# Optimization experiments

Hardware: AMD Instinct MI355X
Metric: run time of the kernel (lower is better)

The kernel has to match this reference:

```python
import jax, jax.numpy as jnp
import numpy as np

B, N, T, F, K = 32, 24, 12, 3, 3
COUT = 12                      # must equal T (LayerNorm applied to last dim = T)
DIN = N * COUT + N + 1         # 313 = lstm_in_dim
H = DIN * T                    # 3756 = lstm_hidden_dim (forced by residual add)
ODIM = 1
LN_EPS = 1e-5


def setup_inputs() -> dict:
    key = jax.random.key(0)
    ks = jax.random.split(key, 24)
    r = lambda i, shape, s=0.1: jax.random.normal(ks[i], shape, dtype=jnp.float32) * s
    return {
        "X": r(0, (B, N, T, F), 1.0),
        "cheb": r(1, (K, N, N), 0.3),
        # Spatial_Attention_layer (ASTGCN-style) params
        "sa_W1": r(2, (T,)), "sa_W2": r(3, (F, T)), "sa_W3": r(4, (F,)),
        "sa_bs": r(5, (1, N, N)), "sa_Vs": r(6, (N, N)),
        # Temporal_Attention_layer params
        "ta_U1": r(7, (N,)), "ta_U2": r(8, (F, N)), "ta_U3": r(9, (F,)),
        "ta_be": r(10, (1, T, T)), "ta_Ve": r(11, (T, T)),
        # ChebConv_with_sa params
        "theta": r(12, (K, F, COUT)), "cheb_bias": jnp.zeros((COUT,), jnp.float32),
        # LayerNorm
        "ln_g": jnp.ones((COUT,), jnp.float32), "ln_b": jnp.zeros((COUT,), jnp.float32),
        # layer_in: Linear(seq_len, seq_len)
        "layer_in_w": r(13, (T, T)), "layer_in_b": r(14, (T,)),
        # S_A2: Linear(lstm_in_dim, lstm_in_dim)
        "sa2_w": r(15, (DIN, DIN), 0.05), "sa2_b": r(16, (DIN,)),
        # LSTMCell (torch gate order i,f,g,o)
        "W_ih": r(17, (4 * H, DIN), 0.02), "W_hh": r(18, (4 * H, H), 0.01),
        "b_ih": jnp.zeros((4 * H,), jnp.float32), "b_hh": jnp.zeros((4 * H,), jnp.float32),
        # T_A2: Linear(seq_len*hidden, seq_len)
        "ta2_w": r(19, (T, T * H), 0.02), "ta2_b": r(20, (T,)),
        # layer_out
        "out_w": r(21, (ODIM, H), 0.02), "out_b": jnp.zeros((ODIM,), jnp.float32),
        # torch.randn initial states (fixed here for determinism)
        "h0": r(22, (B, H), 1.0), "c0": r(23, (B, H), 1.0),
    }


def reference(X, cheb, sa_W1, sa_W2, sa_W3, sa_bs, sa_Vs,
              ta_U1, ta_U2, ta_U3, ta_be, ta_Ve,
              theta, cheb_bias, ln_g, ln_b,
              layer_in_w, layer_in_b, sa2_w, sa2_b,
              W_ih, W_hh, b_ih, b_hh, ta2_w, ta2_b,
              out_w, out_b, h0, c0):
    sig = jax.nn.sigmoid
    Bsz = X.shape[0]
    x_flow = X[:, 0:1, :, 1]                     # (B,1,T)
    x_rain = X[:, :, :, 0]                       # (B,N,T)
    x_pre = jnp.concatenate([x_rain, x_flow], axis=1)  # (B,N+1,T)
    x4 = jnp.transpose(X, (0, 1, 3, 2))          # (B,N,F,T)

    # spatial attention; legacy nn.Softmax() on 3D tensor => axis=0
    lhs = jnp.einsum('bnf,ft->bnt', jnp.einsum('bnft,t->bnf', x4, sa_W1), sa_W2)
    rhs = jnp.einsum('f,bnft->btn', sa_W3, x4)
    S = jnp.einsum('nm,bmk->bnk', sa_Vs, sig(jnp.einsum('bnt,btm->bnm', lhs, rhs) + sa_bs))
    s_a = jax.nn.softmax(sig(jax.nn.softmax(S, axis=1)), axis=0)   # (B,N,N)

    # temporal attention
    xp = jnp.transpose(x4, (0, 3, 2, 1))         # (B,T,F,N)
    lhs_t = jnp.einsum('btf,fn->btn', jnp.einsum('btfn,n->btf', xp, ta_U1), ta_U2)
    rhs_t = jnp.einsum('f,bnft->bnt', ta_U3, x4)
    E = jnp.einsum('tu,buv->btv', ta_Ve, sig(jnp.einsum('btn,bnu->btu', lhs_t, rhs_t) + ta_be))
    t_a = jax.nn.softmax(sig(jax.nn.softmax(E, axis=1)), axis=0)   # (B,T,T)

    # attention-weighted Chebyshev conv; note reshape (not transpose), as in original
    xg = X.reshape(Bsz, N, F, -1)                # (B,N,F,T)
    Tk_at = cheb[None] * s_a[:, None]            # (B,K,N,N)
    rhs_g = jnp.einsum('bkmn,bmft->bknft', Tk_at, xg)
    xc = jax.nn.relu(jnp.einsum('bknft,kfo->bnot', rhs_g, theta) + cheb_bias[:, None])  # (B,N,COUT,T)

    # LayerNorm over last dim (T == COUT)
    mu = xc.mean(-1, keepdims=True)
    var = xc.var(-1, keepdims=True)
    x_ln = (xc - mu) / jnp.sqrt(var + LN_EPS) * ln_g + ln_b

    x_gc = x_ln.reshape(Bsz, -1, 12)             # (B, N*COUT, 12)
    x_gc_t = jnp.einsum('bij,bjk->bik', x_gc, t_a)
    x_res = jnp.concatenate([x_gc_t, x_pre], axis=1)   # (B, DIN, 12)
    x_in = x_res @ layer_in_w.T + layer_in_b     # Linear over last (seq) dim
    xs = jnp.transpose(x_in, (2, 0, 1))          # (T, B, DIN)

    def step(carry, x_t):
        h, c = carry
        alpha = jax.nn.softmax(sig(x_t @ sa2_w.T + sa2_b), axis=1)
        xi = x_t * alpha + x_t
        gates = xi @ W_ih.T + b_ih + h @ W_hh.T + b_hh
        i, f, g, o = jnp.split(gates, 4, axis=1)
        c2 = sig(f) * c + sig(i) * jnp.tanh(g)
        h2 = sig(o) * jnp.tanh(c2)
        return (h2, c2), h2

    _, hs = jax.lax.scan(step, (h0, c0), xs)     # (T,B,H)
    total_ht = jnp.transpose(hs, (1, 0, 2)).reshape(Bsz, -1)  # cat along dim 1, time-major
    beta = jax.nn.softmax(jax.nn.relu(total_ht @ ta2_w.T + ta2_b), axis=1)  # (B,T)
    out = jnp.einsum('tbh,bt->bh', hs, beta)
    out = out + x_in.reshape(Bsz, -1)            # requires H == DIN*T
    out = jax.nn.relu(out) @ out_w.T + out_b
    return out, s_a
```

## Files before the change

kernel.cpp:

```cpp
#include <hip/hip_runtime.h>

#define BSZ 32
#define NN 24
#define TT 12
#define FF 3
#define KK 3
#define COUT 12
#define DIN 313
#define HID 3756
#define H4 15024
#define KP 3776
#define KPI 320
#define NTILES 470
#define NB 235
#define NCH 30

using short8 = __attribute__((ext_vector_type(8))) short;
using f32x4  = __attribute__((ext_vector_type(4))) float;

__device__ inline unsigned short f2bf(float f){
  union{float f; unsigned u;} v; v.f=f;
  unsigned u=v.u;
  return (unsigned short)((u + 0x7FFFu + ((u>>16)&1u))>>16);
}
__device__ inline f32x4 mfma16(short8 a, short8 b, f32x4 c){
  return __builtin_amdgcn_mfma_f32_16x16x32_bf16(a,b,c,0,0,0);
}
__device__ inline float sigm(float x){ return 1.f/(1.f+expf(-x)); }

__device__ void conv_slab(const float* __restrict__ W, unsigned short* __restrict__ Wp,
    int bi, int cg0, int cg1, int tid, int nthr, unsigned short* lds){
  for(int cg=cg0; cg<cg1; cg++){
    int ks0=cg*4;
    int nks=min(4,118-ks0);
    int nf4=nks*8;
    for(int q=tid;q<64*nf4;q+=nthr){
      int r=q/nf4, f4=q-r*nf4;
      int g=r>>4, lj=r&15;
      int jj=bi*16+lj; if(jj>=HID) jj=HID-1;
      const float* src=W+(long)(g*HID+jj)*HID;
      int k=ks0*32+f4*4;
      ushort4 o;
      if(k+3<HID){
        float4 v=*(const float4*)(src+k);
        o.x=f2bf(v.x); o.y=f2bf(v.y); o.z=f2bf(v.z); o.w=f2bf(v.w);
      } else {
        float vv[4];
        #pragma unroll
        for(int t2=0;t2<4;t2++){ int kk=k+t2; vv[t2]=(kk<HID)?src[kk]:0.f; }
        o.x=f2bf(vv[0]); o.y=f2bf(vv[1]); o.z=f2bf(vv[2]); o.w=f2bf(vv[3]);
      }
      *(ushort4*)(&lds[r*136+f4*4])=o;
    }
    __syncthreads();
    for(int idx=tid; idx<nks*4*64; idx+=nthr){
      int l=idx&63, g=(idx>>6)&3, kl=idx>>8;
      int lj=l&15, lk=l>>4;
      short8 v=*(short8*)(&lds[(g*16+lj)*136 + kl*32 + lk*8]);
      *(short8*)(Wp + (((long)(bi*118+ks0+kl)*4+g)*64 + l)*8) = v;
    }
    __syncthreads();
  }
}

__device__ void pack_ih(const float* __restrict__ Wih, unsigned short* __restrict__ Wip,
    int jt, int tid, int nthr, unsigned short* lds ){
  int j0=jt*32;
  for(int q=tid;q<32*80;q+=nthr){
    int r=q/80, f4=q-r*80;
    int j=j0+r;
    int k=f4*4;
    ushort4 o;
    if(j<H4){
      const float* src=Wih+(long)j*DIN;
      float vv[4];
      #pragma unroll
      for(int t2=0;t2<4;t2++){ int kk=k+t2; vv[t2]=(kk<DIN)?src[kk]:0.f; }
      o.x=f2bf(vv[0]); o.y=f2bf(vv[1]); o.z=f2bf(vv[2]); o.w=f2bf(vv[3]);
    } else { o.x=0;o.y=0;o.z=0;o.w=0; }
    *(ushort4*)(&lds[r*328+k])=o;
  }
  __syncthreads();
  for(int u=tid;u<1280;u+=nthr){
    int l=u&63, jh=(u>>6)&1, ks=u>>7;
    int lj=l&15, lk=l>>4;
    short8 v=*(short8*)(&lds[(jh*16+lj)*328 + ks*32 + lk*8]);
    *(short8*)(Wip + (((long)(jt*10+ks)*2+jh)*512) + l*8)=v;
  }
  __syncthreads();
}

__global__ void __launch_bounds__(256) k_f1(const float* __restrict__ X,
   const float* __restrict__ sa_W1, const float* __restrict__ sa_W2,
   const float* __restrict__ sa_W3, const float* __restrict__ sa_bs,
   const float* __restrict__ sa_Vs, const float* __restrict__ ta_U1,
   const float* __restrict__ ta_U2, const float* __restrict__ ta_U3,
   const float* __restrict__ ta_be, const float* __restrict__ ta_Ve,
   float* __restrict__ SA_pre, float* __restrict__ TA_pre,
   const float* __restrict__ W, unsigned short* __restrict__ Wp,
   const float* __restrict__ Wih, unsigned short* __restrict__ Wip){
  __shared__ __align__(16) float smf[5248];
  int tid=threadIdx.x;
  if(blockIdx.x>=267){
    int cb=blockIdx.x-267;
    #pragma unroll
    for(int s=0;s<4;s++){
      int jt=cb*4+s;
      if(jt<NTILES) pack_ih(Wih,Wip,jt,tid,256,(unsigned short*)smf);
    }
    return;
  }
  if(blockIdx.x>=32){
    conv_slab(W,Wp,blockIdx.x-32,0,8,tid,256,(unsigned short*)smf);
    return;
  }
  int b=blockIdx.x;
  float* lin=smf;        float* lhs=smf+864;   float* rhs=smf+1152;
  float* P=smf+1440;     float* S=smf+2016;    float* lhsT=smf+2592;
  float* rhsT=smf+2880;  float* PT=smf+3168;   float* E=smf+3312;
  for(int i=tid;i<864;i+=256) lin[i]=X[b*864+i];
  __syncthreads();
  for(int i=tid;i<NN*TT;i+=256){ int n=i/TT, t=i%TT;
    float acc=0;
    #pragma unroll
    for(int f=0;f<FF;f++){
      float t1=0;
      for(int u=0;u<TT;u++) t1 += lin[n*36+u*3+f]*sa_W1[u];
      acc += t1*sa_W2[f*TT+t];
    }
    lhs[n*TT+t]=acc;
    float r=0;
    #pragma unroll
    for(int f=0;f<FF;f++) r += sa_W3[f]*lin[n*36+t*3+f];
    rhs[t*NN+n]=r;
  }
  for(int i=tid;i<TT*NN;i+=256){ int t=i/NN, n=i%NN;
    float acc=0;
    #pragma unroll
    for(int f=0;f<FF;f++){
      float t1=0;
      for(int m=0;m<NN;m++) t1 += lin[m*36+t*3+f]*ta_U1[m];
      acc += t1*ta_U2[f*NN+n];
    }
    lhsT[t*NN+n]=acc;
    float r=0;
    #pragma unroll
    for(int f=0;f<FF;f++) r += ta_U3[f]*lin[n*36+t*3+f];
    rhsT[n*TT+t]=r;
  }
  __syncthreads();
  for(int i=tid;i<NN*NN;i+=256){ int n=i/NN,m=i%NN;
    float a=0;
    for(int t=0;t<TT;t++) a+=lhs[n*TT+t]*rhs[t*NN+m];
    P[i]=sigm(a+sa_bs[i]);
  }
  for(int i=tid;i<TT*TT;i+=256){ int t=i/TT,u=i%TT;
    float a=0;
    for(int n=0;n<NN;n++) a+=lhsT[t*NN+n]*rhsT[n*TT+u];
    PT[i]=sigm(a+ta_be[i]);
  }
  __syncthreads();
  for(int i=tid;i<NN*NN;i+=256){ int n=i/NN,k=i%NN;
    float a=0;
    for(int m=0;m<NN;m++) a+=sa_Vs[n*NN+m]*P[m*NN+k];
    S[i]=a;
  }
  for(int i=tid;i<TT*TT;i+=256){ int t=i/TT,v=i%TT;
    float a=0;
    for(int u=0;u<TT;u++) a+=ta_Ve[t*TT+u]*PT[u*TT+v];
    E[i]=a;
  }
  __syncthreads();
  if(tid<NN){ int k=tid;
    float mx=-1e30f;
    for(int n=0;n<NN;n++) mx=fmaxf(mx,S[n*NN+k]);
    float sm=0;
    for(int n=0;n<NN;n++) sm+=__expf(S[n*NN+k]-mx);
    for(int n=0;n<NN;n++){
      float v=__expf(S[n*NN+k]-mx)/sm;
      SA_pre[b*576+n*NN+k]=sigm(v);
    }
  }
  if(tid>=32 && tid<32+TT){ int v=tid-32;
    float mx=-1e30f;
    for(int t=0;t<TT;t++) mx=fmaxf(mx,E[t*TT+v]);
    float sm=0;
    for(int t=0;t<TT;t++) sm+=__expf(E[t*TT+v]-mx);
    for(int t=0;t<TT;t++){
      float e=__expf(E[t*TT+v]-mx)/sm;
      TA_pre[b*144+t*TT+v]=sigm(e);
    }
  }
}

__global__ void __launch_bounds__(320) k_f2(const float* __restrict__ X,
  const float* __restrict__ cheb, const float* __restrict__ SA_pre,
  const float* __restrict__ TA_pre, const float* __restrict__ theta,
  const float* __restrict__ cheb_bias, const float* __restrict__ ln_g,
  const float* __restrict__ ln_b, const float* __restrict__ liw,
  const float* __restrict__ lib, float* __restrict__ x_in,
  float* __restrict__ out_sa,
  const float* __restrict__ W, unsigned short* __restrict__ Wp,
  const float* __restrict__ sa2_w, float* __restrict__ sa2_wT){
  __shared__ __align__(16) float smf[13116];
  int tid=threadIdx.x;
  if(blockIdx.x>=267){
    int cb=blockIdx.x-267;
    for(int idx=cb*320+tid; idx<DIN*DIN; idx+=40*320){
      int i=idx/DIN, j=idx-i*DIN;
      sa2_wT[idx]=sa2_w[(long)j*DIN+i];
    }
    return;
  }
  if(blockIdx.x>=32){
    conv_slab(W,Wp,blockIdx.x-32,8,16,tid,320,(unsigned short*)smf);
    return;
  }
  int b=blockIdx.x;
  float* lin =smf;
  float* A2  =smf+864;
  float* rg  =smf+2592;
  float* xc  =smf+5184;
  float* xres=smf+8640;
  float* tal =smf+12396;
  float* sa_l=smf+12540;
  for(int i=tid;i<864;i+=320) lin[i]=X[b*864+i];
  for(int i=tid;i<576;i+=320){
    float mx=-1e30f;
    for(int bb=0;bb<BSZ;bb++) mx=fmaxf(mx,SA_pre[bb*576+i]);
    float sm=0;
    for(int bb=0;bb<BSZ;bb++) sm+=__expf(SA_pre[bb*576+i]-mx);
    float v=__expf(SA_pre[b*576+i]-mx)/sm;
    sa_l[i]=v;
    out_sa[b*576+i]=v;
  }
  for(int i=tid;i<144;i+=320){
    float mx=-1e30f;
    for(int bb=0;bb<BSZ;bb++) mx=fmaxf(mx,TA_pre[bb*144+i]);
    float sm=0;
    for(int bb=0;bb<BSZ;bb++) sm+=__expf(TA_pre[bb*144+i]-mx);
    tal[i]=__expf(TA_pre[b*144+i]-mx)/sm;
  }
  __syncthreads();
  for(int i=tid;i<KK*NN*NN;i+=320){ int mn=i%576; A2[i]=cheb[i]*sa_l[mn]; }
  __syncthreads();
  for(int i=tid;i<KK*NN*FF*TT;i+=320){
    int t=i%TT, f=(i/TT)%FF, n=(i/36)%NN, k=i/864;
    float a=0;
    for(int m=0;m<NN;m++) a+=A2[k*576+m*NN+n]*lin[m*36+f*TT+t];
    rg[i]=a;
  }
  __syncthreads();
  for(int i=tid;i<NN*COUT*TT;i+=320){
    int t=i%TT, o=(i/TT)%COUT, n=i/(COUT*TT);
    float a=cheb_bias[o];
    #pragma unroll
    for(int k=0;k<KK;k++)
      #pragma unroll
      for(int f=0;f<FF;f++)
        a += rg[((k*NN+n)*FF+f)*TT+t]*theta[(k*FF+f)*COUT+o];
    xc[i]=fmaxf(a,0.f);
  }
  __syncthreads();
  if(tid<NN*COUT){
    float mu=0;
    for(int t=0;t<TT;t++) mu+=xc[tid*TT+t];
    mu*=(1.f/12.f);
    float var=0;
    for(int t=0;t<TT;t++){ float d=xc[tid*TT+t]-mu; var+=d*d; }
    var*=(1.f/12.f);
    float inv=rsqrtf(var+1e-5f);
    for(int t=0;t<TT;t++) xc[tid*TT+t]=(xc[tid*TT+t]-mu)*inv*ln_g[t]+ln_b[t];
  }
  __syncthreads();
  for(int i=tid;i<NN*COUT;i+=320){
    for(int v=0;v<TT;v++){
      float a=0;
      for(int t=0;t<TT;t++) a+=xc[i*TT+t]*tal[t*TT+v];
      xres[i*TT+v]=a;
    }
  }
  for(int i=tid;i<25*TT;i+=320){
    int r=i/TT, t=i%TT;
    float v=(r<NN)? lin[r*36+t*3+0] : lin[t*3+1];
    xres[(288+r)*TT+t]=v;
  }
  __syncthreads();
  for(int i=tid;i<DIN;i+=320){
    for(int t=0;t<TT;t++){
      float a=lib[t];
      #pragma unroll
      for(int u=0;u<TT;u++) a+=xres[i*TT+u]*liw[t*TT+u];
      x_in[((long)b*DIN+i)*TT+t]=a;
    }
  }
}

__global__ void __launch_bounds__(512) k_f3(const float* __restrict__ x_in,
    const float* __restrict__ sa2_wT, const float* __restrict__ sa2_b,
    unsigned short* __restrict__ xi_b,
    const float* __restrict__ W, unsigned short* __restrict__ Wp){
  __shared__ __align__(16) float smf[4352];
  int tid=threadIdx.x;
  if(blockIdx.x>=384){
    conv_slab(W,Wp,blockIdx.x-384,16,23,tid,512,(unsigned short*)smf);
    return;
  }
  int blk=blockIdx.x; int t=blk>>5, b=blk&31;
  float* xt=smf;
  float* red=smf+320;
  if(tid<DIN) xt[tid]=x_in[((long)b*DIN+tid)*TT+t];
  __syncthreads();
  float z=-1e30f, e=0.f;
  if(tid<DIN){
    float a=sa2_b[tid];
    for(int i=0;i<DIN;i++) a+=xt[i]*sa2_wT[(long)i*DIN+tid];
    z=sigm(a);
  }
  red[tid]=z; __syncthreads();
  for(int off=256;off>0;off>>=1){ if(tid<off) red[tid]=fmaxf(red[tid],red[tid+off]); __syncthreads(); }
  float mx=red[0]; __syncthreads();
  e=(tid<DIN)?__expf(z-mx):0.f;
  red[tid]=e; __syncthreads();
  for(int off=256;off>0;off>>=1){ if(tid<off) red[tid]+=red[tid+off]; __syncthreads(); }
  float sm=red[0];
  if(tid<KPI){
    unsigned short v=0;
    if(tid<DIN){
      float alpha=e/sm;
      v=f2bf(xt[tid]*alpha+xt[tid]);
    }
    xi_b[(long)blk*KPI+tid]=v;
  }
}

__global__ void __launch_bounds__(256) k_f4(const unsigned short* __restrict__ xi,
   const unsigned short* __restrict__ Wip, const float* __restrict__ b_ih,
   const float* __restrict__ b_hh, float* __restrict__ Gx,
   const float* __restrict__ W, unsigned short* __restrict__ Wp,
   const float* __restrict__ h0f, unsigned short* __restrict__ hb0,
   unsigned short* __restrict__ hb1){
  __shared__ __align__(16) float smf[4352];
  int tid=threadIdx.x;
  if(blockIdx.x>=118){
    int cb_=blockIdx.x-118;
    conv_slab(W,Wp,cb_,23,30,tid,256,(unsigned short*)smf);
    const int g4=KP>>2;
    for(int i=cb_*256+tid; i<BSZ*g4; i+=NB*256){
      int gq=i%g4, r=i/g4;
      int k=gq*4;
      float vv[4];
      if(k+3<HID){
        float4 x=*(const float4*)(h0f+(long)r*HID+k);
        vv[0]=x.x; vv[1]=x.y; vv[2]=x.z; vv[3]=x.w;
      } else {
        #pragma unroll
        for(int q=0;q<4;q++){ int kk=k+q; vv[q]=(kk<HID)? h0f[(long)r*HID+kk] : 0.f; }
      }
      ushort4 o;
      o.x=f2bf(vv[0]); o.y=f2bf(vv[1]); o.z=f2bf(vv[2]); o.w=f2bf(vv[3]);
      *(ushort4*)(hb0+(long)r*KP+k)=o;
      *(ushort4*)(hb1+(long)r*KP+k)=o;
    }
    return;
  }
  int w=tid>>6, lane=tid&63;
  int jt=blockIdx.x*4+w;
  if(jt>=NTILES) return;
  int j0=jt*32;
  int lj=lane&15, lk=lane>>4;
  const unsigned short* wslab = Wip + (long)jt*10240;
  short8 bfr[10][2];
  #pragma unroll
  for(int ks=0;ks<10;ks++)
    #pragma unroll
    for(int jh=0;jh<2;jh++)
      bfr[ks][jh]=*(const short8*)(wslab + ((ks*2+jh)<<9) + (lane<<3));
  for(int t=0;t<TT;t++){
    f32x4 acc[2][2]={};
    #pragma unroll
    for(int ks=0;ks<10;ks++){
      #pragma unroll
      for(int mh=0;mh<2;mh++){
        short8 a=*(const short8*)(xi + ((long)(t*32+mh*16+lj))*KPI + ks*32 + lk*8);
        acc[mh][0]=mfma16(a,bfr[ks][0],acc[mh][0]);
        acc[mh][1]=mfma16(a,bfr[ks][1],acc[mh][1]);
      }
    }
    #pragma unroll
    for(int mh=0;mh<2;mh++)
      #pragma unroll
      for(int jh=0;jh<2;jh++){
        int j=j0+jh*16+lj;
        if(j<H4){
          float bias=b_ih[j]+b_hh[j];
          #pragma unroll
          for(int r=0;r<4;r++){
            int bb=mh*16+lk*4+r;
            Gx[((long)t*32+bb)*H4+j]=acc[mh][jh][r]+bias;
          }
        }
      }
  }
}

__global__ void __launch_bounds__(512) k_step(const unsigned short* __restrict__ hb_r,
    unsigned short* __restrict__ hb_w, const unsigned short* __restrict__ Wp,
    const float* __restrict__ Gx, const float* __restrict__ c0,
    float* __restrict__ c, float* __restrict__ hs, int t){
  const int tid=threadIdx.x;
  const int w=tid>>6, lane=tid&63;
  const int j0=blockIdx.x*16;
  const int lj=lane&15, lk=lane>>4;
  const int s0=(118*w)>>3, s1=(118*(w+1))>>3;
  const unsigned short* slab = Wp + (long)blockIdx.x*64*KP;
  f32x4 acc[4][2]={};
  #pragma unroll 2
  for(int ks=s0;ks<s1;ks++){
    int kofs=ks*32+lk*8;
    short8 a0=*(const short8*)(hb_r + (long)lj*KP + kofs);
    short8 a1=*(const short8*)(hb_r + (long)(16+lj)*KP + kofs);
    const unsigned short* pk = slab + ((long)ks<<11);
    #pragma unroll
    for(int g=0;g<4;g++){
      short8 bv=*(const short8*)(pk + (g<<9) + (lane<<3));
      acc[g][0]=mfma16(a0,bv,acc[g][0]);
      acc[g][1]=mfma16(a1,bv,acc[g][1]);
    }
  }
  __shared__ float red[8][4][512];
  #pragma unroll
  for(int g=0;g<4;g++)
    #pragma unroll
    for(int mh=0;mh<2;mh++)
      #pragma unroll
      for(int r=0;r<4;r++)
        red[w][g][(mh*16+lk*4+r)*16+lj]=acc[g][mh][r];
  __syncthreads();
  if(tid<512){
    int p=tid;
    int bb=p>>4, jl=p&15; int j=j0+jl;
    if(j<HID){
      long gxo=((long)t*BSZ+bb)*H4 + j;
      float si=0,sf=0,sg=0,so=0;
      #pragma unroll
      for(int ww=0;ww<8;ww++){
        si+=red[ww][0][p]; sf+=red[ww][1][p];
        sg+=red[ww][2][p]; so+=red[ww][3][p];
      }
      si+=Gx[gxo]; sf+=Gx[gxo+HID]; sg+=Gx[gxo+2*HID]; so+=Gx[gxo+3*HID];
      float gi=sigm(si), gf=sigm(sf), gg=tanhf(sg), go=sigm(so);
      int idx=bb*HID+j;
      float cin=(t==0)?c0[idx]:c[idx];
      float c2=gf*cin+gi*gg;
      float h2=go*tanhf(c2);
      c[idx]=c2;
      hs[(long)t*BSZ*HID+idx]=h2;
      hb_w[(long)bb*KP+j]=f2bf(h2);
    }
  }
}

__global__ void k_tail(const float* __restrict__ hs, const float* __restrict__ ta2_w,
   const float* __restrict__ ta2_b, const float* __restrict__ x_in,
   const float* __restrict__ out_w, const float* __restrict__ out_b,
   float* __restrict__ out0){
  int b=blockIdx.x, tid=threadIdx.x;
  float p[12]={0,0,0,0,0,0,0,0,0,0,0,0};
  for(int idx=tid; idx<TT*HID; idx+=256){
    int t=idx/HID, j=idx-t*HID;
    float v=hs[((long)t*BSZ+b)*HID+j];
    #pragma unroll
    for(int q=0;q<12;q++) p[q]+=v*ta2_w[(long)q*TT*HID+idx];
  }
  __shared__ float red[256];
  __shared__ float bt[12];
  float z[12];
  #pragma unroll
  for(int q=0;q<12;q++){
    __syncthreads();
    red[tid]=p[q]; __syncthreads();
    for(int off=128;off>0;off>>=1){ if(tid<off) red[tid]+=red[tid+off]; __syncthreads(); }
    z[q]=red[0];
  }
  if(tid==0){
    float mx=-1e30f;
    #pragma unroll
    for(int q=0;q<12;q++){ z[q]=fmaxf(z[q]+ta2_b[q],0.f); mx=fmaxf(mx,z[q]); }
    float sm=0;
    #pragma unroll
    for(int q=0;q<12;q++){ z[q]=__expf(z[q]-mx); sm+=z[q]; }
    #pragma unroll
    for(int q=0;q<12;q++) bt[q]=z[q]/sm;
  }
  __syncthreads();
  float acc=0;
  for(int j=tid;j<HID;j+=256){
    float ov=0;
    #pragma unroll
    for(int t=0;t<TT;t++) ov+=hs[((long)t*BSZ+b)*HID+j]*bt[t];
    ov+=x_in[(long)b*HID+j];
    acc+=fmaxf(ov,0.f)*out_w[j];
  }
  __syncthreads();
  red[tid]=acc; __syncthreads();
  for(int off=128;off>0;off>>=1){ if(tid<off) red[tid]+=red[tid+off]; __syncthreads(); }
  if(tid==0) out0[b]=red[0]+out_b[0];
}

extern "C" void kernel_launch(void* const* d_in, const int* in_sizes, int n_in,
                              void* d_out, int out_size, void* d_ws, size_t ws_size,
                              hipStream_t stream){
  (void)in_sizes; (void)n_in; (void)out_size; (void)ws_size;
  const float* X     =(const float*)d_in[0];
  const float* cheb  =(const float*)d_in[1];
  const float* sa_W1 =(const float*)d_in[2];
  const float* sa_W2 =(const float*)d_in[3];
  const float* sa_W3 =(const float*)d_in[4];
  const float* sa_bs =(const float*)d_in[5];
  const float* sa_Vs =(const float*)d_in[6];
  const float* ta_U1 =(const float*)d_in[7];
  const float* ta_U2 =(const float*)d_in[8];
  const float* ta_U3 =(const float*)d_in[9];
  const float* ta_be =(const float*)d_in[10];
  const float* ta_Ve =(const float*)d_in[11];
  const float* theta =(const float*)d_in[12];
  const float* cb    =(const float*)d_in[13];
  const float* ln_g  =(const float*)d_in[14];
  const float* ln_b  =(const float*)d_in[15];
  const float* liw   =(const float*)d_in[16];
  const float* lib   =(const float*)d_in[17];
  const float* sa2_w =(const float*)d_in[18];
  const float* sa2_b =(const float*)d_in[19];
  const float* W_ih  =(const float*)d_in[20];
  const float* W_hh  =(const float*)d_in[21];
  const float* b_ih  =(const float*)d_in[22];
  const float* b_hh  =(const float*)d_in[23];
  const float* ta2_w =(const float*)d_in[24];
  const float* ta2_b =(const float*)d_in[25];
  const float* out_w =(const float*)d_in[26];
  const float* out_b =(const float*)d_in[27];
  const float* h0    =(const float*)d_in[28];
  const float* c0    =(const float*)d_in[29];

  char* w=(char*)d_ws;
  unsigned short* Wp =(unsigned short*)(w);
  float* Gx   =(float*)(w+113582080);
  float* hs   =(float*)(w+136658944);
  unsigned short* hb0=(unsigned short*)(w+142428160);
  unsigned short* hb1=(unsigned short*)(w+142669824);
  float* c    =(float*)(w+142911488);
  float* x_in =(float*)(w+143392256);
  unsigned short* xi_b=(unsigned short*)(w+143873024);
  float* SA   =(float*)(w+144118784);
  float* TA   =(float*)(w+144192512);
  unsigned short* Wip=(unsigned short*)(w+144211968);
  float* sa2T =(float*)(w+153837568);
  float* out_f=(float*)d_out;

  k_f1<<<385,256,0,stream>>>(X,sa_W1,sa_W2,sa_W3,sa_bs,sa_Vs,ta_U1,ta_U2,ta_U3,ta_be,ta_Ve,
                             SA,TA,W_hh,Wp,W_ih,Wip);
  k_f2<<<307,320,0,stream>>>(X,cheb,SA,TA,theta,cb,ln_g,ln_b,liw,lib,x_in,out_f+32,W_hh,Wp,
                             sa2_w,sa2T);
  k_f3<<<384+NB,512,0,stream>>>(x_in,sa2T,sa2_b,xi_b,W_hh,Wp);
  k_f4<<<118+NB,256,0,stream>>>(xi_b,Wip,b_ih,b_hh,Gx,W_hh,Wp,h0,hb0,hb1);
  unsigned short* hb[2]={hb0,hb1};
  for(int t=0;t<TT;t++)
    k_step<<<NB,512,0,stream>>>(hb[t&1],hb[(t+1)&1],Wp,Gx,c0,c,hs,t);
  k_tail<<<32,256,0,stream>>>(hs,ta2_w,ta2_b,x_in,out_w,out_b,out_f);
}
```

Before: 555.6 us.

## Split per-batch graph-conv kernel into per-(batch,node) blocks plus separate layer_in kernel

The preprocessing kernel previously used one block per batch (32 blocks) for the Chebyshev conv, LayerNorm and temporal attention chain. It is now split into 768 blocks, one per (batch, node), which write an intermediate xres buffer. A new elementwise kernel then applies the layer_in linear. The aim is to fill more compute units and shorten this serial stage, at the cost of an extra kernel launch, a global round-trip for xres, and redundant per-block loads of X and the attention softmax.

Result: no change. 564.0 us (+1.5%).

```diff
diff --git a/kernel.cpp b/kernel.cpp
--- a/kernel.cpp
+++ b/kernel.cpp
@@ -193,48 +193,45 @@
   }
 }
 
-__global__ void __launch_bounds__(320) k_f2(const float* __restrict__ X,
+__global__ void __launch_bounds__(256) k_f2a(const float* __restrict__ X,
   const float* __restrict__ cheb, const float* __restrict__ SA_pre,
   const float* __restrict__ TA_pre, const float* __restrict__ theta,
   const float* __restrict__ cheb_bias, const float* __restrict__ ln_g,
-  const float* __restrict__ ln_b, const float* __restrict__ liw,
-  const float* __restrict__ lib, float* __restrict__ x_in,
+  const float* __restrict__ ln_b, float* __restrict__ xres,
   float* __restrict__ out_sa,
   const float* __restrict__ W, unsigned short* __restrict__ Wp,
   const float* __restrict__ sa2_w, float* __restrict__ sa2_wT){
-  __shared__ __align__(16) float smf[13116];
+  __shared__ __align__(16) float smf[4352];
   int tid=threadIdx.x;
-  if(blockIdx.x>=267){
-    int cb=blockIdx.x-267;
-    for(int idx=cb*320+tid; idx<DIN*DIN; idx+=40*320){
+  if(blockIdx.x>=1003){
+    int cb=blockIdx.x-1003;
+    for(int idx=cb*256+tid; idx<DIN*DIN; idx+=40*256){
       int i=idx/DIN, j=idx-i*DIN;
       sa2_wT[idx]=sa2_w[(long)j*DIN+i];
     }
     return;
   }
-  if(blockIdx.x>=32){
-    conv_slab(W,Wp,blockIdx.x-32,8,16,tid,320,(unsigned short*)smf);
+  if(blockIdx.x>=768){
+    conv_slab(W,Wp,blockIdx.x-768,8,16,tid,256,(unsigned short*)smf);
     return;
   }
-  int b=blockIdx.x;
-  float* lin =smf;
-  float* A2  =smf+864;
-  float* rg  =smf+2592;
-  float* xc  =smf+5184;
-  float* xres=smf+8640;
-  float* tal =smf+12396;
-  float* sa_l=smf+12540;
-  for(int i=tid;i<864;i+=320) lin[i]=X[b*864+i];
-  for(int i=tid;i<576;i+=320){
+  int b=blockIdx.x/NN, n=blockIdx.x%NN;
+  float* lin=smf;
+  float* tal=smf+864;
+  float* sal=smf+1008;
+  float* rg =smf+1032;
+  float* xc =smf+1140;
+  for(int i=tid;i<864;i+=256) lin[i]=X[b*864+i];
+  if(tid<NN){ int m=tid; int mn=m*NN+n;
     float mx=-1e30f;
-    for(int bb=0;bb<BSZ;bb++) mx=fmaxf(mx,SA_pre[bb*576+i]);
+    for(int bb=0;bb<BSZ;bb++) mx=fmaxf(mx,SA_pre[bb*576+mn]);
     float sm=0;
-    for(int bb=0;bb<BSZ;bb++) sm+=__expf(SA_pre[bb*576+i]-mx);
-    float v=__expf(SA_pre[b*576+i]-mx)/sm;
-    sa_l[i]=v;
-    out_sa[b*576+i]=v;
-  }
-  for(int i=tid;i<144;i+=320){
+    for(int bb=0;bb<BSZ;bb++) sm+=__expf(SA_pre[bb*576+mn]-mx);
+    float v=__expf(SA_pre[b*576+mn]-mx)/sm;
+    sal[m]=v;
+    out_sa[b*576+mn]=v;
+  }
+  for(int i=tid;i<144;i+=256){
     float mx=-1e30f;
     for(int bb=0;bb<BSZ;bb++) mx=fmaxf(mx,TA_pre[bb*144+i]);
     float sm=0;
@@ -242,58 +239,65 @@
     tal[i]=__expf(TA_pre[b*144+i]-mx)/sm;
   }
   __syncthreads();
-  for(int i=tid;i<KK*NN*NN;i+=320){ int mn=i%576; A2[i]=cheb[i]*sa_l[mn]; }
-  __syncthreads();
-  for(int i=tid;i<KK*NN*FF*TT;i+=320){
-    int t=i%TT, f=(i/TT)%FF, n=(i/36)%NN, k=i/864;
+  if(tid<108){
+    int k=tid/36, f=(tid/12)%3, t=tid%12;
     float a=0;
-    for(int m=0;m<NN;m++) a+=A2[k*576+m*NN+n]*lin[m*36+f*TT+t];
-    rg[i]=a;
-  }
-  __syncthreads();
-  for(int i=tid;i<NN*COUT*TT;i+=320){
-    int t=i%TT, o=(i/TT)%COUT, n=i/(COUT*TT);
+    for(int m=0;m<NN;m++)
+      a += (cheb[(k*NN+m)*NN+n]*sal[m])*lin[m*36+f*TT+t];
+    rg[tid]=a;
+  }
+  __syncthreads();
+  if(tid<144){
+    int o=tid/12, t=tid%12;
     float a=cheb_bias[o];
     #pragma unroll
     for(int k=0;k<KK;k++)
       #pragma unroll
       for(int f=0;f<FF;f++)
-        a += rg[((k*NN+n)*FF+f)*TT+t]*theta[(k*FF+f)*COUT+o];
-    xc[i]=fmaxf(a,0.f);
-  }
-  __syncthreads();
-  if(tid<NN*COUT){
+        a += rg[k*36+f*12+t]*theta[(k*FF+f)*COUT+o];
+    xc[tid]=fmaxf(a,0.f);
+  }
+  __syncthreads();
+  if(tid<COUT){
+    int o=tid;
     float mu=0;
-    for(int t=0;t<TT;t++) mu+=xc[tid*TT+t];
+    for(int t=0;t<TT;t++) mu+=xc[o*TT+t];
     mu*=(1.f/12.f);
     float var=0;
-    for(int t=0;t<TT;t++){ float d=xc[tid*TT+t]-mu; var+=d*d; }
+    for(int t=0;t<TT;t++){ float d=xc[o*TT+t]-mu; var+=d*d; }
     var*=(1.f/12.f);
     float inv=rsqrtf(var+1e-5f);
-    for(int t=0;t<TT;t++) xc[tid*TT+t]=(xc[tid*TT+t]-mu)*inv*ln_g[t]+ln_b[t];
-  }
-  __syncthreads();
-  for(int i=tid;i<NN*COUT;i+=320){
-    for(int v=0;v<TT;v++){
-      float a=0;
-      for(int t=0;t<TT;t++) a+=xc[i*TT+t]*tal[t*TT+v];
-      xres[i*TT+v]=a;
-    }
-  }
-  for(int i=tid;i<25*TT;i+=320){
-    int r=i/TT, t=i%TT;
-    float v=(r<NN)? lin[r*36+t*3+0] : lin[t*3+1];
-    xres[(288+r)*TT+t]=v;
-  }
-  __syncthreads();
-  for(int i=tid;i<DIN;i+=320){
-    for(int t=0;t<TT;t++){
-      float a=lib[t];
-      #pragma unroll
-      for(int u=0;u<TT;u++) a+=xres[i*TT+u]*liw[t*TT+u];
-      x_in[((long)b*DIN+i)*TT+t]=a;
-    }
-  }
+    for(int t=0;t<TT;t++) xc[o*TT+t]=(xc[o*TT+t]-mu)*inv*ln_g[t]+ln_b[t];
+  }
+  __syncthreads();
+  if(tid<144){
+    int o=tid/12, v=tid%12;
+    float a=0;
+    for(int t=0;t<TT;t++) a+=xc[o*TT+t]*tal[t*TT+v];
+    xres[((long)b*DIN + n*COUT+o)*TT + v]=a;
+  }
+}
+
+__global__ void __launch_bounds__(256) k_f2b(const float* __restrict__ xres,
+    const float* __restrict__ X, const float* __restrict__ liw,
+    const float* __restrict__ lib, float* __restrict__ x_in){
+  int id=blockIdx.x*256+threadIdx.x;
+  if(id>=BSZ*DIN*TT) return;
+  int t=id%TT, i=(id/TT)%DIN, b=id/(DIN*TT);
+  float a=lib[t];
+  if(i<288){
+    const float* xr=xres+((long)b*DIN+i)*TT;
+    #pragma unroll
+    for(int u=0;u<TT;u++) a+=xr[u]*liw[t*TT+u];
+  } else if(i<312){
+    int r=i-288;
+    #pragma unroll
+    for(int u=0;u<TT;u++) a+=X[b*864+r*36+u*3+0]*liw[t*TT+u];
+  } else {
+    #pragma unroll
+    for(int u=0;u<TT;u++) a+=X[b*864+u*3+1]*liw[t*TT+u];
+  }
+  x_in[id]=a;
 }
 
 __global__ void __launch_bounds__(512) k_f3(const float* __restrict__ x_in,
@@ -556,12 +560,14 @@
   float* TA   =(float*)(w+144192512);
   unsigned short* Wip=(unsigned short*)(w+144211968);
   float* sa2T =(float*)(w+153837568);
+  float* xres =(float*)(w+154229504);
   float* out_f=(float*)d_out;
 
   k_f1<<<385,256,0,stream>>>(X,sa_W1,sa_W2,sa_W3,sa_bs,sa_Vs,ta_U1,ta_U2,ta_U3,ta_be,ta_Ve,
                              SA,TA,W_hh,Wp,W_ih,Wip);
-  k_f2<<<307,320,0,stream>>>(X,cheb,SA,TA,theta,cb,ln_g,ln_b,liw,lib,x_in,out_f+32,W_hh,Wp,
-                             sa2_w,sa2T);
+  k_f2a<<<1043,256,0,stream>>>(X,cheb,SA,TA,theta,cb,ln_g,ln_b,xres,out_f+32,W_hh,Wp,
+                               sa2_w,sa2T);
+  k_f2b<<<470,256,0,stream>>>(xres,X,liw,lib,x_in);
   k_f3<<<384+NB,512,0,stream>>>(x_in,sa2T,sa2_b,xi_b,W_hh,Wp);
   k_f4<<<118+NB,256,0,stream>>>(xi_b,Wip,b_ih,b_hh,Gx,W_hh,Wp,h0,hb0,hb1);
   unsigned short* hb[2]={hb0,hb1};
```

## Split tail attention kernel into parallel partial-reduction kernels

Applied to the files above, without the earlier changes.

Replaces the single 32-block tail kernel with four kernels. The first computes the temporal attention projection split across batch, output and chunk (1536 blocks). The second does the softmax, the third computes the weighted sum and output dot product across 256 blocks, and the last reduces the partials. This is meant to remove the under-parallelized tail that used only 32 workgroups, at the cost of extra launches and workspace round trips.

After: 467.1 us. 15.9% less time.

```diff
diff --git a/kernel.cpp b/kernel.cpp
--- a/kernel.cpp
+++ b/kernel.cpp
@@ -461,51 +461,76 @@
   }
 }
 
-__global__ void k_tail(const float* __restrict__ hs, const float* __restrict__ ta2_w,
-   const float* __restrict__ ta2_b, const float* __restrict__ x_in,
-   const float* __restrict__ out_w, const float* __restrict__ out_b,
-   float* __restrict__ out0){
-  int b=blockIdx.x, tid=threadIdx.x;
-  float p[12]={0,0,0,0,0,0,0,0,0,0,0,0};
-  for(int idx=tid; idx<TT*HID; idx+=256){
+__global__ void __launch_bounds__(256) k_t1(const float* __restrict__ hs,
+    const float* __restrict__ ta2_w, float* __restrict__ zpart){
+  int bq=blockIdx.x, s=blockIdx.y, tid=threadIdx.x;
+  int b=bq/12, q=bq-b*12;
+  const int CH=11268;
+  int i0=s*CH, i1=i0+CH;
+  const float* wq=ta2_w+(long)q*45072;
+  float acc=0;
+  for(int idx=i0+tid; idx<i1; idx+=256){
     int t=idx/HID, j=idx-t*HID;
-    float v=hs[((long)t*BSZ+b)*HID+j];
-    #pragma unroll
-    for(int q=0;q<12;q++) p[q]+=v*ta2_w[(long)q*TT*HID+idx];
+    acc+=hs[((long)t*BSZ+b)*HID+j]*wq[idx];
   }
   __shared__ float red[256];
+  red[tid]=acc; __syncthreads();
+  for(int off=128;off>0;off>>=1){ if(tid<off) red[tid]+=red[tid+off]; __syncthreads(); }
+  if(tid==0) zpart[(bq<<2)+s]=red[0];
+}
+
+__global__ void __launch_bounds__(384) k_t2(const float* __restrict__ zpart,
+    const float* __restrict__ ta2_b, float* __restrict__ beta){
+  __shared__ float zz[384];
+  int tid=threadIdx.x;
+  int b=tid/12, q=tid-b*12;
+  float z=zpart[(tid<<2)]+zpart[(tid<<2)+1]+zpart[(tid<<2)+2]+zpart[(tid<<2)+3]+ta2_b[q];
+  zz[tid]=fmaxf(z,0.f);
+  __syncthreads();
+  if(q==0){
+    float mx=-1e30f;
+    #pragma unroll
+    for(int k=0;k<12;k++) mx=fmaxf(mx,zz[b*12+k]);
+    float sm=0;
+    float e[12];
+    #pragma unroll
+    for(int k=0;k<12;k++){ e[k]=__expf(zz[b*12+k]-mx); sm+=e[k]; }
+    #pragma unroll
+    for(int k=0;k<12;k++) beta[b*12+k]=e[k]/sm;
+  }
+}
+
+__global__ void __launch_bounds__(256) k_t3(const float* __restrict__ hs,
+    const float* __restrict__ beta, const float* __restrict__ x_in,
+    const float* __restrict__ out_w, float* __restrict__ opart){
+  int blk=blockIdx.x, tid=threadIdx.x;
+  int b=blk>>3, jc=blk&7;
   __shared__ float bt[12];
-  float z[12];
-  #pragma unroll
-  for(int q=0;q<12;q++){
-    __syncthreads();
-    red[tid]=p[q]; __syncthreads();
-    for(int off=128;off>0;off>>=1){ if(tid<off) red[tid]+=red[tid+off]; __syncthreads(); }
-    z[q]=red[0];
-  }
-  if(tid==0){
-    float mx=-1e30f;
-    #pragma unroll
-    for(int q=0;q<12;q++){ z[q]=fmaxf(z[q]+ta2_b[q],0.f); mx=fmaxf(mx,z[q]); }
-    float sm=0;
-    #pragma unroll
-    for(int q=0;q<12;q++){ z[q]=__expf(z[q]-mx); sm+=z[q]; }
-    #pragma unroll
-    for(int q=0;q<12;q++) bt[q]=z[q]/sm;
-  }
-  __syncthreads();
+  if(tid<12) bt[tid]=beta[b*12+tid];
+  __syncthreads();
+  int j0=jc*470, j1=min(HID,j0+470);
   float acc=0;
-  for(int j=tid;j<HID;j+=256){
+  for(int j=j0+tid;j<j1;j+=256){
     float ov=0;
     #pragma unroll
     for(int t=0;t<TT;t++) ov+=hs[((long)t*BSZ+b)*HID+j]*bt[t];
     ov+=x_in[(long)b*HID+j];
     acc+=fmaxf(ov,0.f)*out_w[j];
   }
-  __syncthreads();
+  __shared__ float red[256];
   red[tid]=acc; __syncthreads();
   for(int off=128;off>0;off>>=1){ if(tid<off) red[tid]+=red[tid+off]; __syncthreads(); }
-  if(tid==0) out0[b]=red[0]+out_b[0];
+  if(tid==0) opart[blk]=red[0];
+}
+
+__global__ void k_t4(const float* __restrict__ opart, const float* __restrict__ out_b,
+    float* __restrict__ out0){
+  int b=threadIdx.x;
+  if(b>=BSZ) return;
+  float a=out_b[0];
+  #pragma unroll
+  for(int jc=0;jc<8;jc++) a+=opart[(b<<3)+jc];
+  out0[b]=a;
 }
 
 extern "C" void kernel_launch(void* const* d_in, const int* in_sizes, int n_in,
@@ -556,6 +581,9 @@
   float* TA   =(float*)(w+144192512);
   unsigned short* Wip=(unsigned short*)(w+144211968);
   float* sa2T =(float*)(w+153837568);
+  float* zpart=(float*)(w+154229504);
+  float* beta =(float*)(w+154235648);
+  float* opart=(float*)(w+154237184);
   float* out_f=(float*)d_out;
 
   k_f1<<<385,256,0,stream>>>(X,sa_W1,sa_W2,sa_W3,sa_bs,sa_Vs,ta_U1,ta_U2,ta_U3,ta_be,ta_Ve,
@@ -567,5 +595,8 @@
   unsigned short* hb[2]={hb0,hb1};
   for(int t=0;t<TT;t++)
     k_step<<<NB,512,0,stream>>>(hb[t&1],hb[(t+1)&1],Wp,Gx,c0,c,hs,t);
-  k_tail<<<32,256,0,stream>>>(hs,ta2_w,ta2_b,x_in,out_w,out_b,out_f);
-}
+  k_t1<<<dim3(384,4),256,0,stream>>>(hs,ta2_w,zpart);
+  k_t2<<<1,384,0,stream>>>(zpart,ta2_b,beta);
+  k_t3<<<256,256,0,stream>>>(hs,beta,x_in,out_w,opart);
+  k_t4<<<1,64,0,stream>>>(opart,out_b,out_f);
+}
```
